# Kernel tuning notes

Measured on AMD Instinct MI355X. Metric: run time of the kernel, lower is better.

Reference implementation:

```python
import jax, jax.numpy as jnp
import numpy as np

H = 1024
L = 4

def _lstm_layer(xs, w_ih, w_hh, b):
    # xs: [B, T, in]; w_ih: [4H, in]; w_hh: [4H, H]; b: [4H] (b_ih + b_hh)
    xp = jnp.einsum('bti,gi->btg', xs, w_ih) + b  # [B, T, 4H]
    xp = jnp.swapaxes(xp, 0, 1)                   # [T, B, 4H]
    B = xs.shape[0]
    h0 = jnp.zeros((B, H), xs.dtype)
    c0 = jnp.zeros((B, H), xs.dtype)

    def step(carry, xp_t):
        h, c = carry
        gates = xp_t + h @ w_hh.T                 # [B, 4H]
        i, f, g, o = jnp.split(gates, 4, axis=-1)  # PyTorch gate order i,f,g,o
        i = jax.nn.sigmoid(i)
        f = jax.nn.sigmoid(f)
        g = jnp.tanh(g)
        o = jax.nn.sigmoid(o)
        c = f * c + i * g
        h = o * jnp.tanh(c)
        return (h, c), h

    (hT, cT), hs = jax.lax.scan(step, (h0, c0), xp)
    return jnp.swapaxes(hs, 0, 1), hT             # [B, T, H], [B, H]


def setup_inputs() -> dict:
    key = jax.random.key(0)
    ks = jax.random.split(key, 8)
    s = 1.0 / np.sqrt(H)
    u = lambda k, shp: jax.random.uniform(k, shp, jnp.float32, -s, s)
    return {
        'x': jax.random.normal(ks[0], (64, 256, 2), jnp.float32),
        'w_ih0': u(ks[1], (4 * H, 2)),            # layer 0 input weights
        'w_ih_rest': u(ks[2], (L - 1, 4 * H, H)), # layers 1..3 input weights
        'w_hh': u(ks[3], (L, 4 * H, H)),
        'b_ih': u(ks[4], (L, 4 * H)),
        'b_hh': u(ks[5], (L, 4 * H)),
        'fc_w': u(ks[6], (1, H)),
        'fc_b': u(ks[7], (1,)),
    }


def reference(x, w_ih0, w_ih_rest, w_hh, b_ih, b_hh, fc_w, fc_b):
    # 4-layer LSTM, batch_first, zero initial states; dropout inactive (eval mode).
    hs, hT = _lstm_layer(x, w_ih0, w_hh[0], b_ih[0] + b_hh[0])
    for l in range(1, L):
        hs, hT = _lstm_layer(hs, w_ih_rest[l - 1], w_hh[l], b_ih[l] + b_hh[l])
    # fc applied to final hidden state of last layer
    return hT @ fc_w.T + fc_b                      # [B, 1]
```

## Files before the change

kernel.cpp:

```cpp
#include <hip/hip_runtime.h>
#include <hip/hip_bf16.h>
#include <hip/hip_fp16.h>


#define H      1024
#define BATCH  64
#define T      256
#define RINGN  8

typedef _Float16 f16x8 __attribute__((ext_vector_type(8)));
typedef _Float16 f16x4 __attribute__((ext_vector_type(4)));
typedef float    f32x4 __attribute__((ext_vector_type(4)));

#define WPACK_HH_SZ  (4ull*64*32*4*64*8*2)
#define WPACK_IH_SZ  (3ull*64*32*4*64*8*2)
#define HRING_OFF    (WPACK_HH_SZ + WPACK_IH_SZ)
#define SLOT_ELEMS   65536
#define SLOT_BYTES   131072ull
#define CNT_INTS     (4*257*16)
#define CNT_BYTES    ((unsigned long long)CNT_INTS*4)

__host__ __device__ __forceinline__ unsigned long long ring_bytes(int nslot) {
  return 4ull*(unsigned)nslot*SLOT_BYTES;
}
__device__ __forceinline__ int cidx(int l, int s) { return (l*257 + s)*16; }
__device__ __forceinline__ int fidx(int l, int w) { return (l*64 + w)*16; }

__device__ __forceinline__ int aslot(int s, int fresh) {
  if (!fresh) return s & 7;
  return (s >= 256) ? 256 : (int)(__brev((unsigned)s) >> 24);
}

__device__ __forceinline__ void wait_eq64(int* p) {
  int it = 0;
  while (__hip_atomic_load(p, __ATOMIC_RELAXED, __HIP_MEMORY_SCOPE_AGENT) < 64) {
    __builtin_amdgcn_s_sleep(1);
    if (++it > 100000000) break;
  }
}

__device__ __forceinline__ void wait_ge(const int* p, int tgt) {
  int it = 0;
  while (__hip_atomic_load(p, __ATOMIC_RELAXED, __HIP_MEMORY_SCOPE_AGENT) < tgt) {
    __builtin_amdgcn_s_sleep(1);
    if (++it > 100000000) break;
  }
}

__device__ __forceinline__ f16x8 load_h8_sc(const _Float16* p) {
  const unsigned long long* q = (const unsigned long long*)p;
  unsigned long long lo = __hip_atomic_load(q,     __ATOMIC_RELAXED, __HIP_MEMORY_SCOPE_AGENT);
  unsigned long long hi = __hip_atomic_load(q + 1, __ATOMIC_RELAXED, __HIP_MEMORY_SCOPE_AGENT);
  union { unsigned long long u[2]; f16x8 v; } c;
  c.u[0] = lo; c.u[1] = hi;
  return c.v;
}

__global__ void pack_kernel(const float* __restrict__ w_ih_rest,
                            const float* __restrict__ w_hh,
                            char* __restrict__ ws, int nslot)
{
  const long long NS_HH = 4ll*64*32*4*64;
  const long long NS_IH = 3ll*64*32*4*64;
  const long long NS_HZ = 4ll*8192;
  const long long NTOT  = NS_HH + NS_IH + NS_HZ + 256;
  _Float16* whh_dst = (_Float16*)ws;
  _Float16* wih_dst = (_Float16*)(ws + WPACK_HH_SZ);
  int* cnt = (int*)(ws + HRING_OFF + ring_bytes(nslot));
  for (long long i = blockIdx.x*(long long)blockDim.x + threadIdx.x; i < NTOT;
       i += (long long)gridDim.x*blockDim.x) {
    if (i < NS_HH + NS_IH) {
      const bool is_hh = (i < NS_HH);
      long long slot = is_hh ? i : (i - NS_HH);
      long long j = slot;
      int lane = (int)(j & 63); j >>= 6;
      int nt   = (int)(j & 3);  j >>= 2;
      int ks   = (int)(j & 31); j >>= 5;
      int wg   = (int)(j & 63); j >>= 6;
      int l    = (int)j;
      int row = nt*1024 + wg*16 + (lane & 15);
      int col = ks*32 + (lane >> 4)*8;
      const float* src = (is_hh ? w_hh : w_ih_rest) + ((long long)l*4096 + row)*1024 + col;
      f16x8 v;
      #pragma unroll
      for (int e = 0; e < 8; e++) v[e] = (_Float16)src[e];
      *(f16x8*)((is_hh ? whh_dst : wih_dst) + slot*8) = v;
    } else if (i < NS_HH + NS_IH + NS_HZ) {
      long long j = i - (NS_HH + NS_IH);
      long long l = j >> 13;
      long long off = j & 8191;
      uint4 z = make_uint4(0,0,0,0);
      ((uint4*)(ws + HRING_OFF))[(l*(long long)nslot)*8192 + off] = z;
    } else {
      int k = (int)(i - (NS_HH + NS_IH + NS_HZ));
      cnt[k*16] = 0;
    }
  }
}

__global__ __launch_bounds__(256, 1) void lstm_main(
    const float* __restrict__ x,
    const float* __restrict__ wih0,
    const float* __restrict__ bih,
    const float* __restrict__ bhh,
    char* __restrict__ ws, int nslot, int fresh)
{
  __builtin_amdgcn_fence(__ATOMIC_ACQUIRE, "agent");

  extern __shared__ char lds[];
  _Float16* whh_lds = (_Float16*)lds;
  _Float16* bufs    = (_Float16*)(lds + 114688);

  const int l   = blockIdx.x >> 6;
  const int wg  = blockIdx.x & 63;
  const int tid = threadIdx.x;
  const int wave = tid >> 6;
  const int lane = tid & 63;

  const _Float16* wpack_hh = (const _Float16*)ws + (size_t)(l*64 + wg)*65536;
  const _Float16* wpack_ih = (l > 0)
      ? (const _Float16*)(ws + WPACK_HH_SZ) + (size_t)((l-1)*64 + wg)*65536
      : wpack_hh;
  _Float16* hring = (_Float16*)(ws + HRING_OFF);
  int* cnt  = (int*)(ws + HRING_OFF + ring_bytes(nslot));
  int* cnt2 = cnt + CNT_INTS;

  {
    const uint4* src = (const uint4*)wpack_hh;
    uint4* dst = (uint4*)whh_lds;
    for (int i = tid; i < 7168; i += 256) dst[i] = src[i];
  }

  const int b_ew = tid >> 2;
  const int u0   = (tid & 3) * 4;
  float cst[4] = {0.f, 0.f, 0.f, 0.f};
  float bias[4][4];
  float wx0[4][4], wx1[4][4];
  #pragma unroll
  for (int ii = 0; ii < 4; ii++) {
    #pragma unroll
    for (int g = 0; g < 4; g++) {
      int row = g*1024 + wg*16 + u0 + ii;
      bias[ii][g] = bih[l*4096 + row] + bhh[l*4096 + row];
      if (l == 0) { wx0[ii][g] = wih0[row*2]; wx1[ii][g] = wih0[row*2 + 1]; }
      else        { wx0[ii][g] = 0.f;         wx1[ii][g] = 0.f; }
    }
  }
  __syncthreads();

  const int m_row = lane & 15, quad = lane >> 4;

  for (int s = 1; s <= T; s++) {
    if (fresh) {
      if (l == 0) {
        if (lane < 16) wait_ge(cnt + fidx(0, wave*16 + lane), s - 1);
      } else {
        if (wave == 0)      { if (lane < 32) wait_ge(cnt + fidx(l-1, lane),      s); }
        else if (wave == 1) { if (lane < 32) wait_ge(cnt + fidx(l-1, 32 + lane), s); }
        else if (wave == 2) { if (lane < 32) wait_ge(cnt + fidx(l,   lane),      s - 1); }
        else                { if (lane < 32) wait_ge(cnt + fidx(l,   32 + lane), s - 1); }
      }
    } else {
      if (wave == 0) {
        wait_ge(cnt + fidx(l, lane), s - 1);
      } else if (wave == 1) {
        if (l > 0) wait_ge(cnt + fidx(l - 1, lane), s);
      } else if (tid == 128) {
        if (l < 3 && s > RINGN) wait_eq64(&cnt2[cidx(l, s-RINGN)]);
      }
      __syncthreads();
    }

    const _Float16* asrc = (l > 0 && wave < 2)
        ? hring + ((size_t)(l-1)*nslot + aslot(s,   fresh))*SLOT_ELEMS
        : hring + ((size_t)l*nslot     + aslot(s-1, fresh))*SLOT_ELEMS;

    f32x4 acc[4][4];
    #pragma unroll
    for (int mt = 0; mt < 4; mt++)
      #pragma unroll
      for (int nt = 0; nt < 4; nt++) acc[mt][nt] = (f32x4){0.f, 0.f, 0.f, 0.f};

    auto kb_lds = [&](int ks, bool plain) {
      const int kb = ks*32 + quad*8;
      f16x8 a[4], bb[4];
      #pragma unroll
      for (int mt = 0; mt < 4; mt++) {
        const _Float16* ap = asrc + (size_t)(mt*16 + m_row)*1024 + kb;
        a[mt] = plain ? *(const f16x8*)ap : load_h8_sc(ap);
      }
      #pragma unroll
      for (int nt = 0; nt < 4; nt++)
        bb[nt] = *(const f16x8*)(whh_lds + ((ks*4 + nt)*64 + lane)*8);
      #pragma unroll
      for (int mt = 0; mt < 4; mt++)
        #pragma unroll
        for (int nt = 0; nt < 4; nt++)
          acc[mt][nt] = __builtin_amdgcn_mfma_f32_16x16x32_f16(a[mt], bb[nt], acc[mt][nt], 0, 0, 0);
    };
    auto kb_glob = [&](int ks, const _Float16* bsrc, bool plain) {
      const int kb = ks*32 + quad*8;
      f16x8 a[4], bb[4];
      #pragma unroll
      for (int mt = 0; mt < 4; mt++) {
        const _Float16* ap = asrc + (size_t)(mt*16 + m_row)*1024 + kb;
        a[mt] = plain ? *(const f16x8*)ap : load_h8_sc(ap);
      }
      #pragma unroll
      for (int nt = 0; nt < 4; nt++)
        bb[nt] = *(const f16x8*)(bsrc + ((size_t)(ks*4 + nt)*64 + lane)*8);
      #pragma unroll
      for (int mt = 0; mt < 4; mt++)
        #pragma unroll
        for (int nt = 0; nt < 4; nt++)
          acc[mt][nt] = __builtin_amdgcn_mfma_f32_16x16x32_f16(a[mt], bb[nt], acc[mt][nt], 0, 0, 0);
    };

    const bool pl = (fresh != 0);
    if (l == 0) {
      if (wave < 3) {
        #pragma unroll 4
        for (int i = 0; i < 8; i++) kb_lds(wave*8 + i, pl);
      } else {
        #pragma unroll 4
        for (int i = 0; i < 4; i++) kb_lds(24 + i, pl);
        #pragma unroll
        for (int i = 0; i < 4; i++) kb_glob(28 + i, wpack_hh, pl);
      }
    } else if (wave < 2) {
      #pragma unroll 4
      for (int i = 0; i < 16; i++) kb_glob(wave*16 + i, wpack_ih, pl);
    } else if (wave == 2) {
      #pragma unroll 4
      for (int i = 0; i < 16; i++) kb_lds(i, pl);
    } else {
      #pragma unroll 4
      for (int i = 0; i < 12; i++) kb_lds(16 + i, pl);
      #pragma unroll
      for (int i = 0; i < 4; i++) kb_glob(28 + i, wpack_hh, pl);
    }

    {
      _Float16* mybuf = bufs + (size_t)wave*4096;
      #pragma unroll
      for (int mt = 0; mt < 4; mt++)
        #pragma unroll
        for (int nt = 0; nt < 4; nt++) {
          f16x4 v;
          #pragma unroll
          for (int e = 0; e < 4; e++) v[e] = (_Float16)acc[mt][nt][e];
          *(f16x4*)(mybuf + ((mt*4 + nt)*64 + lane)*4) = v;
        }
    }
    if (!fresh && tid == 0 && l > 0)
      __hip_atomic_fetch_add(&cnt2[cidx(l-1, s)], 1, __ATOMIC_RELAXED, __HIP_MEMORY_SCOPE_AGENT);
    __syncthreads();

    {
      const int mt = b_ew >> 4, q = (b_ew & 15) >> 2, reg = b_ew & 3;
      float xs0 = 0.f, xs1 = 0.f;
      if (l == 0) {
        xs0 = x[((size_t)b_ew*T + (s-1))*2];
        xs1 = x[((size_t)b_ew*T + (s-1))*2 + 1];
      }
      f16x4 hv;
      #pragma unroll
      for (int ii = 0; ii < 4; ii++) {
        const int u = u0 + ii;
        float pre[4];
        #pragma unroll
        for (int g = 0; g < 4; g++) {
          int idx = ((mt*4 + g)*64 + (u + 16*q))*4 + reg;
          pre[g] = (float)bufs[idx] + (float)bufs[4096 + idx]
                 + (float)bufs[8192 + idx] + (float)bufs[12288 + idx]
                 + bias[ii][g] + wx0[ii][g]*xs0 + wx1[ii][g]*xs1;
        }
        float ig = 1.f/(1.f + __expf(-pre[0]));
        float fg = 1.f/(1.f + __expf(-pre[1]));
        float gg = 2.f/(1.f + __expf(-2.f*pre[2])) - 1.f;
        float og = 1.f/(1.f + __expf(-pre[3]));
        float c  = fg*cst[ii] + ig*gg;
        cst[ii] = c;
        float th = 2.f/(1.f + __expf(-2.f*c)) - 1.f;
        hv[ii] = (_Float16)(og*th);
      }
      _Float16* hdst = hring + ((size_t)l*nslot + aslot(s, fresh))*SLOT_ELEMS
                     + (size_t)b_ew*1024 + wg*16 + u0;
      union { f16x4 v; unsigned long long u; } cv; cv.v = hv;
      __hip_atomic_store((unsigned long long*)hdst, cv.u,
                         __ATOMIC_RELAXED, __HIP_MEMORY_SCOPE_AGENT);
    }
    __syncthreads();
    if (tid == 0)
      __hip_atomic_store(cnt + fidx(l, wg), s,
                         __ATOMIC_RELAXED, __HIP_MEMORY_SCOPE_AGENT);
  }
}

__global__ void fc_kernel(const char* __restrict__ ws,
                          const float* __restrict__ fcw,
                          const float* __restrict__ fcb,
                          float* __restrict__ out, int nslot, int fresh)
{
  const _Float16* h3 = (const _Float16*)(ws + HRING_OFF)
                     + ((size_t)3*nslot + aslot(T, fresh))*SLOT_ELEMS;
  __shared__ float red[256];
  const int tid = threadIdx.x;
  const int b = tid >> 2, p = tid & 3;
  float sum = 0.f;
  for (int j = p*256; j < p*256 + 256; j++)
    sum += fcw[j] * (float)h3[(size_t)b*1024 + j];
  red[tid] = sum;
  __syncthreads();
  if (p == 0)
    out[b] = red[tid] + red[tid+1] + red[tid+2] + red[tid+3] + fcb[0];
}

extern "C" void kernel_launch(void* const* d_in, const int* in_sizes, int n_in,
                              void* d_out, int out_size, void* d_ws, size_t ws_size,
                              hipStream_t stream)
{
  const float* x    = (const float*)d_in[0];
  const float* wih0 = (const float*)d_in[1];
  const float* wihr = (const float*)d_in[2];
  const float* whh  = (const float*)d_in[3];
  const float* bih  = (const float*)d_in[4];
  const float* bhh  = (const float*)d_in[5];
  const float* fcw  = (const float*)d_in[6];
  const float* fcb  = (const float*)d_in[7];
  float* out = (float*)d_out;
  char* ws = (char*)d_ws;
  (void)in_sizes; (void)n_in; (void)out_size;

  const unsigned long long ws_big   = HRING_OFF + ring_bytes(257) + 2*CNT_BYTES;
  const unsigned long long ws_small = HRING_OFF + ring_bytes(8)   + 2*CNT_BYTES;
  if (ws_size < ws_small) return;
  const int fresh = (ws_size >= ws_big) ? 1 : 0;
  const int nslot = fresh ? 257 : 8;

  hipFuncSetAttribute(reinterpret_cast<const void*>(lstm_main),
                      hipFuncAttributeMaxDynamicSharedMemorySize, 147456);

  hipMemsetAsync(ws + HRING_OFF + ring_bytes(nslot), 0, (size_t)(2*CNT_BYTES), stream);
  pack_kernel<<<512, 256, 0, stream>>>(wihr, whh, ws, nslot);
  lstm_main<<<256, 256, 147456, stream>>>(x, wih0, bih, bhh, ws, nslot, fresh);
  fc_kernel<<<1, 256, 0, stream>>>(ws, fcw, fcb, out, nslot, fresh);
}
```

Before: 3.423 ms.

## Replace workgroup barriers with per-wave LDS and global flags, rebalance K-slices

Each wave now publishes its own per-step completion counter and polls four counters per producer, which removes the block-wide barriers around the gate reduction and the h store. The partial-sum buffer is double-buffered by step parity so waves can run ahead by one step. The LDS-resident slice of W_hh is shrunk and the K-slices are interleaved across waves so the LDS and global weight reads are spread more evenly. Counter zeroing is dropped from the pack kernel, which risks stale counters unless they are reset elsewhere, and the extra polling adds memory traffic.

```diff
diff --git a/kernel.cpp b/kernel.cpp
--- a/kernel.cpp
+++ b/kernel.cpp
@@ -20,6 +20,12 @@
 #define CNT_INTS     (4*257*16)
 #define CNT_BYTES    ((unsigned long long)CNT_INTS*4)
 
+#define WHH_LDS_KS     18
+#define WHH_LDS_BYTES  (WHH_LDS_KS*4*64*16)
+#define PART_OFF       WHH_LDS_BYTES
+#define FLG_OFF        (PART_OFF + 65536)
+#define LDS_TOTAL      (FLG_OFF + 512)
+
 __host__ __device__ __forceinline__ unsigned long long ring_bytes(int nslot) {
   return 4ull*(unsigned)nslot*SLOT_BYTES;
 }
@@ -39,11 +45,23 @@
   }
 }
 
-__device__ __forceinline__ void wait_ge(const int* p, int tgt) {
+__device__ __forceinline__ void wait_all4_ge(const int* p, int tgt) {
   int it = 0;
-  while (__hip_atomic_load(p, __ATOMIC_RELAXED, __HIP_MEMORY_SCOPE_AGENT) < tgt) {
+  for (;;) {
+    int v0 = __hip_atomic_load(p + 0, __ATOMIC_RELAXED, __HIP_MEMORY_SCOPE_AGENT);
+    int v1 = __hip_atomic_load(p + 1, __ATOMIC_RELAXED, __HIP_MEMORY_SCOPE_AGENT);
+    int v2 = __hip_atomic_load(p + 2, __ATOMIC_RELAXED, __HIP_MEMORY_SCOPE_AGENT);
+    int v3 = __hip_atomic_load(p + 3, __ATOMIC_RELAXED, __HIP_MEMORY_SCOPE_AGENT);
+    if (v0 >= tgt && v1 >= tgt && v2 >= tgt && v3 >= tgt) break;
     __builtin_amdgcn_s_sleep(1);
-    if (++it > 100000000) break;
+    if (++it > 50000000) break;
+  }
+}
+
+__device__ __forceinline__ void lds_wait_ge(const int* p, int tgt) {
+  int it = 0;
+  while (__hip_atomic_load(p, __ATOMIC_ACQUIRE, __HIP_MEMORY_SCOPE_WORKGROUP) < tgt) {
+    if (++it > 200000000) break;
   }
 }
 
@@ -63,10 +81,9 @@
   const long long NS_HH = 4ll*64*32*4*64;
   const long long NS_IH = 3ll*64*32*4*64;
   const long long NS_HZ = 4ll*8192;
-  const long long NTOT  = NS_HH + NS_IH + NS_HZ + 256;
+  const long long NTOT  = NS_HH + NS_IH + NS_HZ;
   _Float16* whh_dst = (_Float16*)ws;
   _Float16* wih_dst = (_Float16*)(ws + WPACK_HH_SZ);
-  int* cnt = (int*)(ws + HRING_OFF + ring_bytes(nslot));
   for (long long i = blockIdx.x*(long long)blockDim.x + threadIdx.x; i < NTOT;
        i += (long long)gridDim.x*blockDim.x) {
     if (i < NS_HH + NS_IH) {
@@ -85,15 +102,12 @@
       #pragma unroll
       for (int e = 0; e < 8; e++) v[e] = (_Float16)src[e];
       *(f16x8*)((is_hh ? whh_dst : wih_dst) + slot*8) = v;
-    } else if (i < NS_HH + NS_IH + NS_HZ) {
+    } else {
       long long j = i - (NS_HH + NS_IH);
       long long l = j >> 13;
       long long off = j & 8191;
       uint4 z = make_uint4(0,0,0,0);
       ((uint4*)(ws + HRING_OFF))[(l*(long long)nslot)*8192 + off] = z;
-    } else {
-      int k = (int)(i - (NS_HH + NS_IH + NS_HZ));
-      cnt[k*16] = 0;
     }
   }
 }
@@ -109,7 +123,8 @@
 
   extern __shared__ char lds[];
   _Float16* whh_lds = (_Float16*)lds;
-  _Float16* bufs    = (_Float16*)(lds + 114688);
+  _Float16* bufs    = (_Float16*)(lds + PART_OFF);
+  int*      ldsflg  = (int*)(lds + FLG_OFF);
 
   const int l   = blockIdx.x >> 6;
   const int wg  = blockIdx.x & 63;
@@ -128,7 +143,8 @@
   {
     const uint4* src = (const uint4*)wpack_hh;
     uint4* dst = (uint4*)whh_lds;
-    for (int i = tid; i < 7168; i += 256) dst[i] = src[i];
+    for (int i = tid; i < WHH_LDS_BYTES/16; i += 256) dst[i] = src[i];
+    if (tid < 8) ldsflg[tid*16] = 0;
   }
 
   const int b_ew = tid >> 2;
@@ -151,20 +167,27 @@
   const int m_row = lane & 15, quad = lane >> 4;
 
   for (int s = 1; s <= T; s++) {
+    const int par = s & 1;
+
     if (fresh) {
       if (l == 0) {
-        if (lane < 16) wait_ge(cnt + fidx(0, wave*16 + lane), s - 1);
+        if (lane < 16) {
+          int wg2 = 2*(wave + 4*(lane >> 1)) + (lane & 1);
+          wait_all4_ge(cnt + fidx(0, wg2), s - 1);
+        }
+      } else if (wave < 2) {
+        if (lane < 32) wait_all4_ge(cnt + fidx(l-1, wave*32 + lane), s);
       } else {
-        if (wave == 0)      { if (lane < 32) wait_ge(cnt + fidx(l-1, lane),      s); }
-        else if (wave == 1) { if (lane < 32) wait_ge(cnt + fidx(l-1, 32 + lane), s); }
-        else if (wave == 2) { if (lane < 32) wait_ge(cnt + fidx(l,   lane),      s - 1); }
-        else                { if (lane < 32) wait_ge(cnt + fidx(l,   32 + lane), s - 1); }
+        if (lane < 32) {
+          int wg2 = 4*(lane >> 1) + (lane & 1) + 2*(wave - 2);
+          wait_all4_ge(cnt + fidx(l, wg2), s - 1);
+        }
       }
     } else {
       if (wave == 0) {
-        wait_ge(cnt + fidx(l, lane), s - 1);
+        wait_all4_ge(cnt + fidx(l, lane), s - 1);
       } else if (wave == 1) {
-        if (l > 0) wait_ge(cnt + fidx(l - 1, lane), s);
+        if (l > 0) wait_all4_ge(cnt + fidx(l - 1, lane), s);
       } else if (tid == 128) {
         if (l < 3 && s > RINGN) wait_eq64(&cnt2[cidx(l, s-RINGN)]);
       }
@@ -218,30 +241,30 @@
 
     const bool pl = (fresh != 0);
     if (l == 0) {
-      if (wave < 3) {
+      if (wave < 2) {
         #pragma unroll 4
-        for (int i = 0; i < 8; i++) kb_lds(wave*8 + i, pl);
+        for (int i = 0; i < 5; i++) kb_lds(4*i + wave, pl);
+        #pragma unroll
+        for (int i = 5; i < 8; i++) kb_glob(4*i + wave, wpack_hh, pl);
       } else {
         #pragma unroll 4
-        for (int i = 0; i < 4; i++) kb_lds(24 + i, pl);
-        #pragma unroll
-        for (int i = 0; i < 4; i++) kb_glob(28 + i, wpack_hh, pl);
+        for (int i = 0; i < 4; i++) kb_lds(4*i + wave, pl);
+        #pragma unroll 4
+        for (int i = 4; i < 8; i++) kb_glob(4*i + wave, wpack_hh, pl);
       }
     } else if (wave < 2) {
       #pragma unroll 4
       for (int i = 0; i < 16; i++) kb_glob(wave*16 + i, wpack_ih, pl);
-    } else if (wave == 2) {
+    } else {
+      const int o = wave - 2;
       #pragma unroll 4
-      for (int i = 0; i < 16; i++) kb_lds(i, pl);
-    } else {
-      #pragma unroll 4
-      for (int i = 0; i < 12; i++) kb_lds(16 + i, pl);
-      #pragma unroll
-      for (int i = 0; i < 4; i++) kb_glob(28 + i, wpack_hh, pl);
+      for (int i = 0; i < 9; i++) kb_lds(2*i + o, pl);
+      #pragma unroll
+      for (int i = 9; i < 16; i++) kb_glob(2*i + o, wpack_hh, pl);
     }
 
     {
-      _Float16* mybuf = bufs + (size_t)wave*4096;
+      _Float16* mybuf = bufs + ((size_t)par*4 + wave)*4096;
       #pragma unroll
       for (int mt = 0; mt < 4; mt++)
         #pragma unroll
@@ -252,11 +275,21 @@
           *(f16x4*)(mybuf + ((mt*4 + nt)*64 + lane)*4) = v;
         }
     }
-    if (!fresh && tid == 0 && l > 0)
-      __hip_atomic_fetch_add(&cnt2[cidx(l-1, s)], 1, __ATOMIC_RELAXED, __HIP_MEMORY_SCOPE_AGENT);
-    __syncthreads();
+
+    if (fresh) {
+      if (lane == 0)
+        __hip_atomic_store(ldsflg + (par*4 + wave)*16, s,
+                           __ATOMIC_RELEASE, __HIP_MEMORY_SCOPE_WORKGROUP);
+      if (lane < 4)
+        lds_wait_ge(ldsflg + (par*4 + lane)*16, s);
+    } else {
+      if (tid == 0 && l > 0)
+        __hip_atomic_fetch_add(&cnt2[cidx(l-1, s)], 1, __ATOMIC_RELAXED, __HIP_MEMORY_SCOPE_AGENT);
+      __syncthreads();
+    }
 
     {
+      const _Float16* base = bufs + (size_t)par*4*4096;
       const int mt = b_ew >> 4, q = (b_ew & 15) >> 2, reg = b_ew & 3;
       float xs0 = 0.f, xs1 = 0.f;
       if (l == 0) {
@@ -271,8 +304,8 @@
         #pragma unroll
         for (int g = 0; g < 4; g++) {
           int idx = ((mt*4 + g)*64 + (u + 16*q))*4 + reg;
-          pre[g] = (float)bufs[idx] + (float)bufs[4096 + idx]
-                 + (float)bufs[8192 + idx] + (float)bufs[12288 + idx]
+          pre[g] = (float)base[idx] + (float)base[4096 + idx]
+                 + (float)base[8192 + idx] + (float)base[12288 + idx]
                  + bias[ii][g] + wx0[ii][g]*xs0 + wx1[ii][g]*xs1;
         }
         float ig = 1.f/(1.f + __expf(-pre[0]));
@@ -290,10 +323,20 @@
       __hip_atomic_store((unsigned long long*)hdst, cv.u,
                          __ATOMIC_RELAXED, __HIP_MEMORY_SCOPE_AGENT);
     }
-    __syncthreads();
-    if (tid == 0)
-      __hip_atomic_store(cnt + fidx(l, wg), s,
-                         __ATOMIC_RELAXED, __HIP_MEMORY_SCOPE_AGENT);
+
+    if (fresh) {
+      if (lane == 0)
+        __hip_atomic_store(cnt + fidx(l, wg) + wave, s,
+                           __ATOMIC_RELEASE, __HIP_MEMORY_SCOPE_AGENT);
+    } else {
+      __syncthreads();
+      if (tid == 0) {
+        __hip_atomic_store(cnt + fidx(l, wg) + 0, s, __ATOMIC_RELAXED, __HIP_MEMORY_SCOPE_AGENT);
+        __hip_atomic_store(cnt + fidx(l, wg) + 1, s, __ATOMIC_RELAXED, __HIP_MEMORY_SCOPE_AGENT);
+        __hip_atomic_store(cnt + fidx(l, wg) + 2, s, __ATOMIC_RELAXED, __HIP_MEMORY_SCOPE_AGENT);
+        __hip_atomic_store(cnt + fidx(l, wg) + 3, s, __ATOMIC_RELAXED, __HIP_MEMORY_SCOPE_AGENT);
+      }
+    }
   }
 }
 
```

Result: slower. 8.873 ms (+159.2%).
